# Kernel optimization log

Measured on AMD Instinct MI355X. Metric: run time of the kernel, lower is better.

## Reference

```python
import jax, jax.numpy as jnp
import numpy as np

B = 64        # num_groups
G = 32        # group_size
D = 2000      # output dim (counts per bin/gene)
M = 16        # m_samples
E = 16        # noise_dim
DIN = 256
LAM = 1.0
TRUST = 0.25
SMOOTH = 1e-8
IPF_ITERS = 60
EPS = 1e-12


def _arch(x, noise, W, b):
    # simple linear architecture: concat(x, noise) @ W + b
    return jnp.concatenate([x, noise], axis=-1) @ W + b


def _loss(x, target, W, b, noise_loss):
    # replicate each row m times (unsqueeze(1).expand(...).reshape == repeat)
    x_rep = jnp.repeat(x, M, axis=0)                      # [n*M, DIN]
    pred = _arch(x_rep, noise_loss, W, b)                 # [n*M, D] (no act_fn in loss path)
    pred = pred.reshape(B, G, M, D).sum(axis=1)           # [B, M, D]
    term_conf = jnp.linalg.norm(pred - target[:, None, :], axis=2).mean(axis=1)  # [B]
    sq = jnp.sum(pred * pred, axis=2)                     # [B, M]
    inn = jnp.einsum('bmd,bnd->bmn', pred, pred)          # [B, M, M]
    sqd = jnp.clip(sq[:, :, None] + sq[:, None, :] - 2.0 * inn, 1e-6)
    d = jnp.sqrt(sqd)
    mask = 1.0 - jnp.eye(M, dtype=d.dtype)
    mean_pd = jnp.sum(d * mask, axis=(1, 2)) / (M * (M - 1))
    return jnp.mean(term_conf - (LAM / 2.0) * mean_pd)


def _ipf(x_pred, C):
    # KL/I-projection with row anchoring (keep_rows=True, trust_clip=0.25)
    y = jnp.clip(x_pred, 0.0)
    C = jnp.clip(C.astype(y.dtype), 0.0)
    R = y.sum(axis=2)                                     # [B, G] anchor row totals
    col_zero = (y.sum(axis=1) <= 0) & (C > 0)
    y = y + SMOOTH * col_zero[:, None, :].astype(y.dtype)
    row_zero = (y.sum(axis=2) <= 0) & (R > 0)
    y = y + SMOOTH * row_zero[:, :, None].astype(y.dtype)

    def body(_, y):
        col = jnp.clip(y.sum(axis=1), EPS)
        y = y * jnp.clip(C / col, 1.0 - TRUST, 1.0 + TRUST)[:, None, :]
        row = jnp.clip(y.sum(axis=2), EPS)
        y = y * jnp.clip(R / row, 1.0 - TRUST, 1.0 + TRUST)[:, :, None]
        return y

    y = jax.lax.fori_loop(0, IPF_ITERS, body, y)
    col = jnp.clip(y.sum(axis=1), EPS)
    return y * (C / col)[:, None, :]


def _rank(v, descending):
    # rank along last axis via double argsort (0 = first picked)
    order = jnp.argsort(-v if descending else v, axis=-1)
    return jnp.argsort(order, axis=-1)


def _round_to_targets(x, target_bd):
    # exact integerization across G per (B, D); jit-safe full-G rank replaces dynamic-k topk+scatter
    x = jnp.clip(x, 0.0)
    xf = jnp.floor(x)
    y = xf.astype(jnp.int32)                              # [B, G, D]
    frac = x - xf
    need = target_bd - y.sum(axis=1)                      # [B, D]
    pos = jnp.clip(need, 0)
    q = pos // G
    y = y + q[:, None, :]
    r = pos - q * G
    rank = _rank(jnp.transpose(frac, (0, 2, 1)), descending=True)   # [B, D, G]
    add = (rank < r[:, :, None]).astype(jnp.int32)
    y = y + jnp.transpose(add, (0, 2, 1))
    # negative residuals: remove from smallest frac among y > 0
    need = target_bd - y.sum(axis=1)
    neg = jnp.clip(-need, 0)
    neg = jnp.minimum(neg, y.sum(axis=1))
    q = neg // G
    y_before = y
    y = jnp.clip(y - q[:, None, :], 0)
    removed = (y_before - y).sum(axis=1)
    r = neg - removed
    frac_m = jnp.where(y > 0, frac, jnp.inf)
    rank = _rank(jnp.transpose(frac_m, (0, 2, 1)), descending=False)
    rem = (rank < r[:, :, None]).astype(jnp.int32)
    y = jnp.clip(y - jnp.transpose(rem, (0, 2, 1)), 0)
    return y


def setup_inputs() -> dict:
    key = jax.random.key(0)
    ks = jax.random.split(key, 6)
    x = jax.random.normal(ks[0], (B * G, DIN), dtype=jnp.float32)
    target = jax.random.uniform(ks[1], (B, D), dtype=jnp.float32) * 100.0
    target_sum = jax.random.randint(ks[2], (B, D), 0, 200, dtype=jnp.int32)
    W = jax.random.normal(ks[3], (DIN + E, D), dtype=jnp.float32) * 0.02
    b = jnp.zeros((D,), dtype=jnp.float32)
    noise_loss = jax.random.normal(ks[4], (B * G * M, E), dtype=jnp.float32)
    noise_sample = jax.random.normal(ks[5], (B * G, E), dtype=jnp.float32)
    return {"x": x, "target": target, "target_sum": target_sum, "W": W, "b": b,
            "noise_loss": noise_loss, "noise_sample": noise_sample}


def reference(x, target, target_sum, W, b, noise_loss, noise_sample):
    loss = _loss(x, target, W, b, noise_loss)
    # conditional_sample pipeline (no-grad in original): softplus act (min_value==0)
    x_pred = jax.nn.softplus(_arch(x, noise_sample, W, b)).reshape(B, G, D)
    y_float = _ipf(x_pred, target_sum.astype(jnp.float32))
    y_int = _round_to_targets(y_float, target_sum.astype(jnp.int32))
    return loss, y_int.reshape(B * G, D)
```

## Files before the change

### kernel.cpp

```cpp
#include <hip/hip_runtime.h>
#include <math.h>

#define NB   64
#define NG   32
#define ND   2000
#define NM   16
#define NE   16
#define NDIN 256
#define NK   272

__device__ __forceinline__ float clampf(float v, float lo, float hi) {
    return fminf(fmaxf(v, lo), hi);
}

__device__ __forceinline__ float softplusf(float v) {
    return (v > 20.f) ? v : log1pf(expf(v));
}

__device__ __forceinline__ float readlane_f(float v, int lane) {
    return __int_as_float(__builtin_amdgcn_readlane(__float_as_int(v), lane));
}

__device__ __forceinline__ float wave_sum32(float v[NG], int lane) {
    {   const bool hi = (lane & 32) != 0;
        #pragma unroll
        for (int k = 0; k < 16; ++k) {
            float s = hi ? v[k] : v[k + 16];
            float r = __shfl_xor(s, 32);
            v[k] = (hi ? v[k + 16] : v[k]) + r;
        }
    }
    {   const bool hi = (lane & 16) != 0;
        #pragma unroll
        for (int k = 0; k < 8; ++k) {
            float s = hi ? v[k] : v[k + 8];
            float r = __shfl_xor(s, 16);
            v[k] = (hi ? v[k + 8] : v[k]) + r;
        }
    }
    {   const bool hi = (lane & 8) != 0;
        #pragma unroll
        for (int k = 0; k < 4; ++k) {
            float s = hi ? v[k] : v[k + 4];
            float r = __shfl_xor(s, 8);
            v[k] = (hi ? v[k + 4] : v[k]) + r;
        }
    }
    {   const bool hi = (lane & 4) != 0;
        #pragma unroll
        for (int k = 0; k < 2; ++k) {
            float s = hi ? v[k] : v[k + 2];
            float r = __shfl_xor(s, 4);
            v[k] = (hi ? v[k + 2] : v[k]) + r;
        }
    }
    {   const bool hi = (lane & 2) != 0;
        float s = hi ? v[0] : v[1];
        float r = __shfl_xor(s, 2);
        v[0] = (hi ? v[1] : v[0]) + r;
    }
    v[0] += __shfl_xor(v[0], 1);
    return v[0];
}


__device__ __forceinline__ void ipf_path(
        const float* __restrict__ xp, const int* __restrict__ tsum,
        float* __restrict__ out, float* smem, int b, int t) {
    const int lane = t & 63, w = t >> 6;
    const int d0 = t * 4;
    const bool valid = (d0 < ND);
    const int g_own = (lane >> 1) & 31;

    float* wred = smem;

    float y0r[4][NG];
    #pragma unroll
    for (int g = 0; g < NG; ++g) {
        float4 v = make_float4(0.f, 0.f, 0.f, 0.f);
        if (valid) v = *(const float4*)(xp + (size_t)(b * NG + g) * ND + d0);
        y0r[0][g] = fmaxf(v.x, 0.f);
        y0r[1][g] = fmaxf(v.y, 0.f);
        y0r[2][g] = fmaxf(v.z, 0.f);
        y0r[3][g] = fmaxf(v.w, 0.f);
    }
    float Cc[4] = {0.f, 0.f, 0.f, 0.f};
    if (valid) {
        const int4 ci = *(const int4*)(tsum + (size_t)b * ND + d0);
        Cc[0] = (float)ci.x; Cc[1] = (float)ci.y; Cc[2] = (float)ci.z; Cc[3] = (float)ci.w;
    }
    float Ac[4] = {1.f, 1.f, 1.f, 1.f};
    float Bown = 1.f;
    float Rown;

    {
        float v[NG];
        #pragma unroll
        for (int g = 0; g < NG; ++g)
            v[g] = y0r[0][g] + y0r[1][g] + y0r[2][g] + y0r[3][g];
        const float tot = wave_sum32(v, lane);
        if ((lane & 1) == 0) wred[w * NG + g_own] = tot;
        __syncthreads();
        float s = 0.f;
        #pragma unroll
        for (int w2 = 0; w2 < 8; ++w2) s += wred[w2 * NG + g_own];
        Rown = s;
    }

    for (int q = 1; q <= 60; ++q) {
        float s0 = 0.f, s1 = 0.f, s2 = 0.f, s3 = 0.f;
        #pragma unroll
        for (int g = 0; g < NG; ++g) {
            const float bg = readlane_f(Bown, 2 * g);
            s0 += y0r[0][g] * bg; s1 += y0r[1][g] * bg;
            s2 += y0r[2][g] * bg; s3 += y0r[3][g] * bg;
        }
        Ac[0] *= clampf(Cc[0] / fmaxf(Ac[0] * s0, 1e-12f), 0.75f, 1.25f);
        Ac[1] *= clampf(Cc[1] / fmaxf(Ac[1] * s1, 1e-12f), 0.75f, 1.25f);
        Ac[2] *= clampf(Cc[2] / fmaxf(Ac[2] * s2, 1e-12f), 0.75f, 1.25f);
        Ac[3] *= clampf(Cc[3] / fmaxf(Ac[3] * s3, 1e-12f), 0.75f, 1.25f);
        float v[NG];
        #pragma unroll
        for (int g = 0; g < NG; ++g)
            v[g] = y0r[0][g] * Ac[0] + y0r[1][g] * Ac[1]
                 + y0r[2][g] * Ac[2] + y0r[3][g] * Ac[3];
        const float tot = wave_sum32(v, lane);
        const int buf = (q & 1) * (8 * NG);
        if ((lane & 1) == 0) wred[buf + w * NG + g_own] = tot;
        __syncthreads();
        float s = 0.f;
        #pragma unroll
        for (int w2 = 0; w2 < 8; ++w2) s += wred[buf + w2 * NG + g_own];
        Bown *= clampf(Rown / fmaxf(Bown * s, 1e-12f), 0.75f, 1.25f);
    }

    if (!valid) return;

    unsigned pk[NG];
    #pragma unroll
    for (int g = 0; g < NG; ++g) pk[g] = 0u;

    #pragma unroll
    for (int j = 0; j < 4; ++j) {
        float fr[NG];
        int   yv[NG];
        float s = 0.f;
        #pragma unroll
        for (int g = 0; g < NG; ++g) {
            const float z = y0r[j][g] * Ac[j] * readlane_f(Bown, 2 * g);
            fr[g] = z;
            s += z;
        }
        const float F = Cc[j] / fmaxf(s, 1e-12f);
        int isum = 0;
        #pragma unroll
        for (int g = 0; g < NG; ++g) {
            const float y = fr[g] * F;
            const float fl = floorf(y);
            yv[g] = (int)fl;
            fr[g] = y - fl;
            isum += yv[g];
        }
        const int Ci = (int)Cc[j];
        const int need = Ci - isum;
        const int pos = max(need, 0);
        const int q = pos >> 5;
        const int r = pos & 31;
        #pragma unroll
        for (int g = 0; g < NG; ++g) yv[g] += q;
        #pragma unroll
        for (int g = 0; g < NG; ++g) {
            int rank = 0;
            #pragma unroll
            for (int h = 0; h < NG; ++h) {
                if (h == g) continue;
                rank += (h < g) ? (fr[h] >= fr[g] ? 1 : 0) : (fr[h] > fr[g] ? 1 : 0);
            }
            if (rank < r) yv[g] += 1;
        }
        int neg = max(-need, 0);
        neg = min(neg, isum);
        if (__builtin_expect(neg > 0, 0)) {
            const int q2 = neg >> 5;
            int removed = 0;
            #pragma unroll
            for (int g = 0; g < NG; ++g) {
                const int yb = yv[g];
                const int yn = max(yb - q2, 0);
                removed += yb - yn;
                yv[g] = yn;
            }
            const int r2 = neg - removed;
            if (r2 > 0) {
                const float INF = __builtin_inff();
                #pragma unroll
                for (int g = 0; g < NG; ++g) {
                    const float fg = (yv[g] > 0) ? fr[g] : INF;
                    int rank = 0;
                    #pragma unroll
                    for (int h = 0; h < NG; ++h) {
                        if (h == g) continue;
                        const float fh = (yv[h] > 0) ? fr[h] : INF;
                        rank += (h < g) ? (fh <= fg ? 1 : 0) : (fh < fg ? 1 : 0);
                    }
                    if (rank < r2) yv[g] = max(yv[g] - 1, 0);
                }
            }
        }
        #pragma unroll
        for (int g = 0; g < NG; ++g)
            pk[g] |= ((unsigned)yv[g]) << (8 * j);
    }
    #pragma unroll
    for (int g = 0; g < NG; ++g) {
        float* op = &out[1 + (size_t)(b * NG + g) * ND + d0];
        op[0] = (float)(pk[g] & 0xffu);
        op[1] = (float)((pk[g] >> 8) & 0xffu);
        op[2] = (float)((pk[g] >> 16) & 0xffu);
        op[3] = (float)((pk[g] >> 24) & 0xffu);
    }
}

__device__ __forceinline__ void loss_path(
        const float* __restrict__ x, const float* __restrict__ nl,
        const float* __restrict__ tgt, const float* __restrict__ W,
        const float* __restrict__ bias, float* __restrict__ res2,
        float* smem, int cx, int b, int t) {
    float* xsl = smem;
    float* nsl = smem + 256;
    float* tgl = smem + 512;
    float* pt  = smem + 764;

    if (t < 256) {
        const float* xb = x + (size_t)b * NG * NDIN;
        float s = 0.f;
        for (int g = 0; g < NG; ++g) s += xb[g * NDIN + t];
        xsl[t] = s;
        const float* nb = nl + (size_t)b * NG * (NM * NE);
        float s2 = 0.f;
        for (int g = 0; g < NG; ++g) s2 += nb[g * (NM * NE) + t];
        nsl[t] = s2;
    }

    int tm = 0, tn = 0;
    if (t >= 16 && t < 152) {
        int p = t - 16;
        for (int m = 0; m < NM; ++m) {
            int c = NM - m;
            if (p < c) { tm = m; tn = m + p; break; }
            p -= c;
        }
    }
    __syncthreads();

    const int d = cx * 250 + t;
    if (t < 250) {
        tgl[t] = tgt[b * ND + d];
        float xw = 0.f;
        #pragma unroll 8
        for (int k = 0; k < NDIN; ++k) xw += xsl[k] * W[(size_t)k * ND + d];
        float we[NE];
        #pragma unroll
        for (int e = 0; e < NE; ++e) we[e] = W[(size_t)(NDIN + e) * ND + d];
        const float base0 = xw + (float)NG * bias[d];
        #pragma unroll
        for (int m = 0; m < NM; ++m) {
            float pm = base0;
            #pragma unroll
            for (int e = 0; e < NE; ++e) pm += nsl[m * NE + e] * we[e];
            pt[m * 252 + t] = pm;
        }
    }
    if (t < 32) {
        pt[(t >> 1) * 252 + 250 + (t & 1)] = 0.f;
        if (t < 2) tgl[250 + t] = 0.f;
    }
    __syncthreads();

    float acc = 0.f;
    if (t < 16) {
        const float4* pa  = (const float4*)&pt[t * 252];
        const float4* tga = (const float4*)&tgl[0];
        for (int i = 0; i < 63; ++i) {
            float4 pv = pa[i], tv = tga[i];
            float e0 = pv.x - tv.x, e1 = pv.y - tv.y, e2 = pv.z - tv.z, e3 = pv.w - tv.w;
            acc += e0 * e0 + e1 * e1 + e2 * e2 + e3 * e3;
        }
    } else if (t < 152) {
        const float4* pa = (const float4*)&pt[tm * 252];
        const float4* pb = (const float4*)&pt[tn * 252];
        for (int i = 0; i < 63; ++i) {
            float4 u = pa[i], v = pb[i];
            acc += u.x * v.x + u.y * v.y + u.z * v.z + u.w * v.w;
        }
    }
    if (t < 152) res2[((size_t)b * 8 + cx) * 152 + t] = acc;
}

extern "C" __global__ __launch_bounds__(512, 1)
void mega(const float* __restrict__ x, const float* __restrict__ nl,
          const float* __restrict__ tgt, const float* __restrict__ W,
          const float* __restrict__ bias, const float* __restrict__ xp,
          const int* __restrict__ tsum, float* __restrict__ out,
          float* __restrict__ res2) {
    __shared__ float smem[4800];
    const int bid = blockIdx.x;
    const int t = threadIdx.x;
    if (bid < NB) {
        ipf_path(xp, tsum, out, smem, bid, t);
    } else {
        const int q = bid - NB;
        loss_path(x, nl, tgt, W, bias, res2, smem, q & 7, q >> 3, t);
    }
}

extern "C" __global__ __launch_bounds__(64)
void k2b_combine(const float* __restrict__ res2, float* __restrict__ out) {
    const int b = blockIdx.x, t = threadIdx.x;
    __shared__ float res[152];
    for (int tau = t; tau < 152; tau += 64) {
        float s = 0.f;
        #pragma unroll
        for (int c = 0; c < 8; ++c) s += res2[((size_t)b * 8 + c) * 152 + tau];
        res[tau] = s;
    }
    __syncthreads();
    if (t == 0) {
        float conf = 0.f;
        for (int m = 0; m < NM; ++m) conf += sqrtf(res[m]);
        conf *= (1.f / NM);
        float pd = 0.f;
        for (int m = 0; m < NM; ++m) {
            const int offm = 16 + m * NM - m * (m - 1) / 2;
            const float sqm = res[offm];
            for (int n = m + 1; n < NM; ++n) {
                const int offn = 16 + n * NM - n * (n - 1) / 2;
                const float sqn = res[offn];
                const float inn = res[offm + (n - m)];
                pd += sqrtf(fmaxf(sqm + sqn - 2.f * inn, 1e-6f));
            }
        }
        pd = 2.f * pd / (float)(NM * (NM - 1));
        atomicAdd(out, (conf - 0.5f * pd) * (1.f / NB));
    }
}

extern "C" __global__ __launch_bounds__(256)
void k3_xpred(const float* __restrict__ x, const float* __restrict__ nsamp,
              const float* __restrict__ W, const float* __restrict__ bias,
              float* __restrict__ xp) {
    const int dx = blockIdx.x;
    const int rb = blockIdx.y;
    const int t  = threadIdx.x;
    __shared__ float xr[8][NK];
    #pragma unroll
    for (int r = 0; r < 8; ++r) {
        const int row = rb * 8 + r;
        xr[r][t] = x[(size_t)row * NDIN + t];
        if (t < NE) xr[r][NDIN + t] = nsamp[row * NE + t];
    }
    __syncthreads();
    if (t >= 250) return;
    const int d = dx * 1000 + 4 * t;
    float acc[8][4];
    #pragma unroll
    for (int r = 0; r < 8; ++r) {
        acc[r][0] = 0.f; acc[r][1] = 0.f; acc[r][2] = 0.f; acc[r][3] = 0.f;
    }
    for (int k = 0; k < NK; k += 4) {
        float4 w[4];
        #pragma unroll
        for (int kk = 0; kk < 4; ++kk) w[kk] = *(const float4*)&W[(size_t)(k + kk) * ND + d];
        #pragma unroll
        for (int r = 0; r < 8; ++r) {
            const float4 xv = *(const float4*)&xr[r][k];
            acc[r][0] += xv.x * w[0].x + xv.y * w[1].x + xv.z * w[2].x + xv.w * w[3].x;
            acc[r][1] += xv.x * w[0].y + xv.y * w[1].y + xv.z * w[2].y + xv.w * w[3].y;
            acc[r][2] += xv.x * w[0].z + xv.y * w[1].z + xv.z * w[2].z + xv.w * w[3].z;
            acc[r][3] += xv.x * w[0].w + xv.y * w[1].w + xv.z * w[2].w + xv.w * w[3].w;
        }
    }
    const float4 bv = *(const float4*)&bias[d];
    #pragma unroll
    for (int r = 0; r < 8; ++r) {
        float4 o;
        o.x = softplusf(acc[r][0] + bv.x);
        o.y = softplusf(acc[r][1] + bv.y);
        o.z = softplusf(acc[r][2] + bv.z);
        o.w = softplusf(acc[r][3] + bv.w);
        *(float4*)&xp[(size_t)(rb * 8 + r) * ND + d] = o;
    }
}

extern "C" void kernel_launch(void* const* d_in, const int* in_sizes, int n_in,
                              void* d_out, int out_size, void* d_ws, size_t ws_size,
                              hipStream_t stream) {
    const float* x     = (const float*)d_in[0];
    const float* tgt   = (const float*)d_in[1];
    const int*   tsum  = (const int*)d_in[2];
    const float* W     = (const float*)d_in[3];
    const float* bias  = (const float*)d_in[4];
    const float* nl    = (const float*)d_in[5];
    const float* nsamp = (const float*)d_in[6];
    float* out = (float*)d_out;
    float* xp  = (float*)d_ws;

    (void)in_sizes; (void)n_in; (void)out_size; (void)ws_size;

    const size_t XPB = (size_t)2048 * 2000 * 4;
    float* res2 = (float*)((char*)d_ws + XPB);

    hipMemsetAsync(d_out, 0, sizeof(float), stream);

    hipLaunchKernelGGL(k3_xpred, dim3(2, 256), dim3(256), 0, stream,
                       x, nsamp, W, bias, xp);
    hipLaunchKernelGGL(mega, dim3(NB + 512), dim3(512), 0, stream,
                       x, nl, tgt, W, bias, xp, tsum, out, res2);
    hipLaunchKernelGGL(k2b_combine, dim3(NB), dim3(64), 0, stream, res2, out);
}
```

Measured before the change: 316.7 us.

## Fuse x_pred GEMM into mega kernel with per-group atomic counter handoff

Moves the x_pred softplus GEMM into the mega kernel as 256 leading blocks, each producing 8 rows across all columns. Each block signals completion through a per-group atomic counter, and the IPF blocks spin on an acquire load until their group's four producer blocks are done. This removes one kernel launch and the inter-kernel barrier so that IPF work can start per group and the loss blocks can overlap with the GEMM. It adds a memset, relies on producer blocks being scheduled before consumers to avoid deadlock, and has spinning blocks occupying CUs while they wait.

```diff
diff --git a/kernel.cpp b/kernel.cpp
--- a/kernel.cpp
+++ b/kernel.cpp
@@ -64,15 +64,73 @@
 }
 
 
+__device__ __forceinline__ void xpred_path(
+        const float* __restrict__ x, const float* __restrict__ nsamp,
+        const float* __restrict__ W, const float* __restrict__ bias,
+        float* __restrict__ xp, int* __restrict__ cnt,
+        float* smem, int rb, int t) {
+    float* xr = smem;
+    #pragma unroll
+    for (int r = 0; r < 8; ++r) {
+        const int row = rb * 8 + r;
+        if (t < 256)      xr[r * NK + t] = x[(size_t)row * NDIN + t];
+        else if (t < NK)  xr[r * NK + t] = nsamp[row * NE + (t - 256)];
+    }
+    __syncthreads();
+    const int d = 4 * t;
+    if (d < ND) {
+        float acc[8][4];
+        #pragma unroll
+        for (int r = 0; r < 8; ++r) {
+            acc[r][0] = 0.f; acc[r][1] = 0.f; acc[r][2] = 0.f; acc[r][3] = 0.f;
+        }
+        for (int k = 0; k < NK; k += 4) {
+            float4 w[4];
+            #pragma unroll
+            for (int kk = 0; kk < 4; ++kk)
+                w[kk] = *(const float4*)&W[(size_t)(k + kk) * ND + d];
+            #pragma unroll
+            for (int r = 0; r < 8; ++r) {
+                const float4 xv = *(const float4*)&xr[r * NK + k];
+                acc[r][0] += xv.x * w[0].x + xv.y * w[1].x + xv.z * w[2].x + xv.w * w[3].x;
+                acc[r][1] += xv.x * w[0].y + xv.y * w[1].y + xv.z * w[2].y + xv.w * w[3].y;
+                acc[r][2] += xv.x * w[0].z + xv.y * w[1].z + xv.z * w[2].z + xv.w * w[3].z;
+                acc[r][3] += xv.x * w[0].w + xv.y * w[1].w + xv.z * w[2].w + xv.w * w[3].w;
+            }
+        }
+        const float4 bv = *(const float4*)&bias[d];
+        #pragma unroll
+        for (int r = 0; r < 8; ++r) {
+            float4 o;
+            o.x = softplusf(acc[r][0] + bv.x);
+            o.y = softplusf(acc[r][1] + bv.y);
+            o.z = softplusf(acc[r][2] + bv.z);
+            o.w = softplusf(acc[r][3] + bv.w);
+            *(float4*)&xp[(size_t)(rb * 8 + r) * ND + d] = o;
+        }
+    }
+    __syncthreads();
+    __threadfence();
+    if (t == 0) atomicAdd(&cnt[rb >> 2], 1);
+}
+
 __device__ __forceinline__ void ipf_path(
         const float* __restrict__ xp, const int* __restrict__ tsum,
-        float* __restrict__ out, float* smem, int b, int t) {
+        float* __restrict__ out, const int* __restrict__ cnt,
+        float* smem, int b, int t) {
     const int lane = t & 63, w = t >> 6;
     const int d0 = t * 4;
     const bool valid = (d0 < ND);
     const int g_own = (lane >> 1) & 31;
 
     float* wred = smem;
+
+    {
+        const int* cb = &cnt[b];
+        while (__hip_atomic_load(cb, __ATOMIC_ACQUIRE,
+                                 __HIP_MEMORY_SCOPE_AGENT) < 4)
+            __builtin_amdgcn_s_sleep(16);
+    }
 
     float y0r[4][NG];
     #pragma unroll
@@ -300,16 +358,19 @@
 extern "C" __global__ __launch_bounds__(512, 1)
 void mega(const float* __restrict__ x, const float* __restrict__ nl,
           const float* __restrict__ tgt, const float* __restrict__ W,
-          const float* __restrict__ bias, const float* __restrict__ xp,
-          const int* __restrict__ tsum, float* __restrict__ out,
-          float* __restrict__ res2) {
+          const float* __restrict__ bias, const float* __restrict__ nsamp,
+          float* __restrict__ xp, const int* __restrict__ tsum,
+          float* __restrict__ out, float* __restrict__ res2,
+          int* __restrict__ cnt) {
     __shared__ float smem[4800];
     const int bid = blockIdx.x;
     const int t = threadIdx.x;
-    if (bid < NB) {
-        ipf_path(xp, tsum, out, smem, bid, t);
+    if (bid < 256) {
+        xpred_path(x, nsamp, W, bias, xp, cnt, smem, bid, t);
+    } else if (bid < 256 + NB) {
+        ipf_path(xp, tsum, out, cnt, smem, bid - 256, t);
     } else {
-        const int q = bid - NB;
+        const int q = bid - (256 + NB);
         loss_path(x, nl, tgt, W, bias, res2, smem, q & 7, q >> 3, t);
     }
 }
@@ -345,53 +406,6 @@
     }
 }
 
-extern "C" __global__ __launch_bounds__(256)
-void k3_xpred(const float* __restrict__ x, const float* __restrict__ nsamp,
-              const float* __restrict__ W, const float* __restrict__ bias,
-              float* __restrict__ xp) {
-    const int dx = blockIdx.x;
-    const int rb = blockIdx.y;
-    const int t  = threadIdx.x;
-    __shared__ float xr[8][NK];
-    #pragma unroll
-    for (int r = 0; r < 8; ++r) {
-        const int row = rb * 8 + r;
-        xr[r][t] = x[(size_t)row * NDIN + t];
-        if (t < NE) xr[r][NDIN + t] = nsamp[row * NE + t];
-    }
-    __syncthreads();
-    if (t >= 250) return;
-    const int d = dx * 1000 + 4 * t;
-    float acc[8][4];
-    #pragma unroll
-    for (int r = 0; r < 8; ++r) {
-        acc[r][0] = 0.f; acc[r][1] = 0.f; acc[r][2] = 0.f; acc[r][3] = 0.f;
-    }
-    for (int k = 0; k < NK; k += 4) {
-        float4 w[4];
-        #pragma unroll
-        for (int kk = 0; kk < 4; ++kk) w[kk] = *(const float4*)&W[(size_t)(k + kk) * ND + d];
-        #pragma unroll
-        for (int r = 0; r < 8; ++r) {
-            const float4 xv = *(const float4*)&xr[r][k];
-            acc[r][0] += xv.x * w[0].x + xv.y * w[1].x + xv.z * w[2].x + xv.w * w[3].x;
-            acc[r][1] += xv.x * w[0].y + xv.y * w[1].y + xv.z * w[2].y + xv.w * w[3].y;
-            acc[r][2] += xv.x * w[0].z + xv.y * w[1].z + xv.z * w[2].z + xv.w * w[3].z;
-            acc[r][3] += xv.x * w[0].w + xv.y * w[1].w + xv.z * w[2].w + xv.w * w[3].w;
-        }
-    }
-    const float4 bv = *(const float4*)&bias[d];
-    #pragma unroll
-    for (int r = 0; r < 8; ++r) {
-        float4 o;
-        o.x = softplusf(acc[r][0] + bv.x);
-        o.y = softplusf(acc[r][1] + bv.y);
-        o.z = softplusf(acc[r][2] + bv.z);
-        o.w = softplusf(acc[r][3] + bv.w);
-        *(float4*)&xp[(size_t)(rb * 8 + r) * ND + d] = o;
-    }
-}
-
 extern "C" void kernel_launch(void* const* d_in, const int* in_sizes, int n_in,
                               void* d_out, int out_size, void* d_ws, size_t ws_size,
                               hipStream_t stream) {
@@ -403,18 +417,19 @@
     const float* nl    = (const float*)d_in[5];
     const float* nsamp = (const float*)d_in[6];
     float* out = (float*)d_out;
-    float* xp  = (float*)d_ws;
 
     (void)in_sizes; (void)n_in; (void)out_size; (void)ws_size;
 
-    const size_t XPB = (size_t)2048 * 2000 * 4;
+    const size_t XPB  = (size_t)2048 * 2000 * 4;
+    const size_t RESB = (size_t)NB * 8 * 152 * 4;
+    float* xp   = (float*)d_ws;
     float* res2 = (float*)((char*)d_ws + XPB);
+    int*   cnt  = (int*)((char*)d_ws + XPB + RESB);
 
     hipMemsetAsync(d_out, 0, sizeof(float), stream);
-
-    hipLaunchKernelGGL(k3_xpred, dim3(2, 256), dim3(256), 0, stream,
-                       x, nsamp, W, bias, xp);
-    hipLaunchKernelGGL(mega, dim3(NB + 512), dim3(512), 0, stream,
-                       x, nl, tgt, W, bias, xp, tsum, out, res2);
+    hipMemsetAsync(cnt, 0, NB * sizeof(int), stream);
+
+    hipLaunchKernelGGL(mega, dim3(256 + NB + 512), dim3(512), 0, stream,
+                       x, nl, tgt, W, bias, nsamp, xp, tsum, out, res2, cnt);
     hipLaunchKernelGGL(k2b_combine, dim3(NB), dim3(64), 0, stream, res2, out);
 }
```

Result: slower. 350.0 us (+10.5%).
